# Optimization experiments

Hardware: AMD Instinct MI355X
Metric: run time of the kernel (lower is better)

The kernel has to match this reference:

```python
import jax, jax.numpy as jnp
import numpy as np

R, C, DIN, E, NREG = 1024, 8192, 16, 5, 2048

def setup_inputs() -> dict:
    key = jax.random.key(0)
    k1, k2, k3, k4, k5 = jax.random.split(key, 5)
    return {
        "region_cell_embedding": jax.random.normal(k1, (R, C, DIN), dtype=jnp.float32),
        "regions_oi": jax.random.randint(k2, (R,), 0, NREG, dtype=jnp.int64),
        "W1": jax.random.normal(k3, (NREG, DIN, E), dtype=jnp.float32) / np.sqrt(DIN),
        "b1": jax.random.normal(k4, (NREG, E), dtype=jnp.float32) * 0.1,
        "Wf": jax.random.normal(k5, (NREG, E, 1), dtype=jnp.float32) / np.sqrt(E),
    }

def reference(region_cell_embedding, regions_oi, W1, b1, Wf):
    # region_cell_embedding: [R, C, DIN]; each region r uses weights W1[regions_oi[r]]
    w = W1[regions_oi]                      # [R, DIN, E] gathered per-region weights
    b = b1[regions_oi]                      # [R, E]
    h = jnp.einsum('rci,rie->rce', region_cell_embedding, w) + b[:, None, :]
    h = jax.nn.gelu(h, approximate=False)   # torch.nn.GELU default is exact (erf)
    wf = Wf[regions_oi]                     # [R, E, 1], final MultiLinear has no bias
    out = jnp.einsum('rce,reo->rco', h, wf)[..., 0]  # [R, C]
    return out.T                            # [C, R] (cells x regions)
```

## Files before the change

### kernel.cpp

```cpp
#include <hip/hip_runtime.h>
#include <math.h>

#define RDIM 1024
#define CDIM 8192
#define DIN  16
#define EDIM 5

#define RT   16
#define CT   256
#define WROW 96

__device__ __forceinline__ float gelu_fast(float x) {
    float x2 = x * x;
    float w  = fmaf(0.044715f, x2, 1.0f);
    float t  = x * w;
    float e  = __builtin_amdgcn_exp2f(-2.3022078f * t);
    float s  = __builtin_amdgcn_rcpf(1.0f + e);
    return x * s;
}

__global__ __launch_bounds__(256)
void e2e_kernel(const float* __restrict__ emb,
                const int*   __restrict__ gidx,
                const float* __restrict__ W1,
                const float* __restrict__ b1,
                const float* __restrict__ Wf,
                float* __restrict__ out)
{
    __shared__ int   s_g[RT];
    __shared__ float s_w[RT * WROW];
    __shared__ float s_tile[CT * (RT + 1)];

    const int tid = threadIdx.x;
    const int c0  = blockIdx.x * CT;
    const int r0  = blockIdx.y * RT;

    if (tid < RT) s_g[tid] = gidx[r0 + tid];
    __syncthreads();

    for (int idx = tid; idx < RT * 90; idx += 256) {
        int rl = idx / 90;
        int k  = idx - rl * 90;
        int g  = s_g[rl];
        float v; int dst;
        if (k < 80)      { v = W1[g * 80 + k];       dst = k;     }
        else if (k < 85) { v = b1[g * 5 + (k - 80)]; dst = k;     }
        else             { v = Wf[g * 5 + (k - 85)]; dst = k + 3; }
        s_w[rl * WROW + dst] = v;
    }
    __syncthreads();

    const int lane = tid & 63;
    const int wv   = tid >> 6;

    #pragma unroll 1
    for (int q = 0; q < 4; ++q) {
        const int rl = wv * 4 + q;
        const int r  = r0 + rl;

        const float4* wp = (const float4*)(s_w + rl * WROW);
        float ww[80], bb[EDIM], wf[EDIM];
        #pragma unroll
        for (int q4 = 0; q4 < 20; ++q4) ((float4*)ww)[q4] = wp[q4];
        {
            float4 bt = wp[20];
            bb[0] = bt.x; bb[1] = bt.y; bb[2] = bt.z; bb[3] = bt.w;
            bb[4] = s_w[rl * WROW + 84];
            float4 ft = wp[22];
            wf[0] = ft.x; wf[1] = ft.y; wf[2] = ft.z; wf[3] = ft.w;
            wf[4] = s_w[rl * WROW + 92];
        }

        #pragma unroll
        for (int m = 0; m < 4; ++m) {
            const int cl = lane + 64 * m;
            const int c  = c0 + cl;
            const float4* p = (const float4*)(emb + ((size_t)r * CDIM + c) * DIN);
            float4 x0 = p[0], x1 = p[1], x2 = p[2], x3 = p[3];
            float x[DIN] = { x0.x, x0.y, x0.z, x0.w,
                             x1.x, x1.y, x1.z, x1.w,
                             x2.x, x2.y, x2.z, x2.w,
                             x3.x, x3.y, x3.z, x3.w };
            float acc = 0.f;
            #pragma unroll
            for (int e = 0; e < EDIM; ++e) {
                float h = bb[e];
                #pragma unroll
                for (int i = 0; i < DIN; ++i)
                    h = fmaf(x[i], ww[i * EDIM + e], h);
                h = gelu_fast(h);
                acc = fmaf(h, wf[e], acc);
            }
            s_tile[cl * (RT + 1) + rl] = acc;
        }
    }
    __syncthreads();

    const int orl  = tid & 15;
    const int ocl0 = tid >> 4;
    #pragma unroll
    for (int it = 0; it < 16; ++it) {
        const int cl = ocl0 + 16 * it;
        out[(size_t)(c0 + cl) * RDIM + r0 + orl] = s_tile[cl * (RT + 1) + orl];
    }
}

extern "C" void kernel_launch(void* const* d_in, const int* in_sizes, int n_in,
                              void* d_out, int out_size, void* d_ws, size_t ws_size,
                              hipStream_t stream) {
    const float* emb  = (const float*)d_in[0];
    const int*   gidx = (const int*)d_in[1];
    const float* W1   = (const float*)d_in[2];
    const float* b1   = (const float*)d_in[3];
    const float* Wf   = (const float*)d_in[4];
    float* out = (float*)d_out;

    dim3 grid(CDIM / CT, RDIM / RT);
    dim3 block(256);
    e2e_kernel<<<grid, block, 0, stream>>>(emb, gidx, W1, b1, Wf, out);
}
```

Before: 819.4 us.

## Split each cell's input across four lanes with float4 coalesced loads and shuffle reduction

Each cell's 16-element input is now spread across four lanes, each loading one float4, so consecutive lanes read consecutive memory. Partial dot products are combined with cross-lane shuffles, and each lane keeps only 20 weights instead of 80. This targets uncoalesced strided loads and high register pressure. In exchange it adds shuffles and computes GELU redundantly on four lanes per cell.

```diff
diff --git a/kernel.cpp b/kernel.cpp
--- a/kernel.cpp
+++ b/kernel.cpp
@@ -1,5 +1,4 @@
 #include <hip/hip_runtime.h>
-#include <math.h>
 
 #define RDIM 1024
 #define CDIM 8192
@@ -12,8 +11,7 @@
 
 __device__ __forceinline__ float gelu_fast(float x) {
     float x2 = x * x;
-    float w  = fmaf(0.044715f, x2, 1.0f);
-    float t  = x * w;
+    float t  = x * fmaf(0.044715f, x2, 1.0f);
     float e  = __builtin_amdgcn_exp2f(-2.3022078f * t);
     float s  = __builtin_amdgcn_rcpf(1.0f + e);
     return x * s;
@@ -52,46 +50,51 @@
 
     const int lane = tid & 63;
     const int wv   = tid >> 6;
+    const int q4   = lane & 3;
+    const int quad = lane >> 2;
 
     #pragma unroll 1
     for (int q = 0; q < 4; ++q) {
         const int rl = wv * 4 + q;
         const int r  = r0 + rl;
 
-        const float4* wp = (const float4*)(s_w + rl * WROW);
-        float ww[80], bb[EDIM], wf[EDIM];
+        const float4* wp4 = (const float4*)(s_w + rl * WROW + q4 * 20);
+        float wl[20];
         #pragma unroll
-        for (int q4 = 0; q4 < 20; ++q4) ((float4*)ww)[q4] = wp[q4];
+        for (int t = 0; t < 5; ++t) ((float4*)wl)[t] = wp4[t];
+        float bb[EDIM], wf[EDIM];
         {
-            float4 bt = wp[20];
+            const float* wr = s_w + rl * WROW;
+            float4 bt = *(const float4*)(wr + 80);
             bb[0] = bt.x; bb[1] = bt.y; bb[2] = bt.z; bb[3] = bt.w;
-            bb[4] = s_w[rl * WROW + 84];
-            float4 ft = wp[22];
+            bb[4] = wr[84];
+            float4 ft = *(const float4*)(wr + 88);
             wf[0] = ft.x; wf[1] = ft.y; wf[2] = ft.z; wf[3] = ft.w;
-            wf[4] = s_w[rl * WROW + 92];
+            wf[4] = wr[92];
         }
 
-        #pragma unroll
-        for (int m = 0; m < 4; ++m) {
-            const int cl = lane + 64 * m;
-            const int c  = c0 + cl;
-            const float4* p = (const float4*)(emb + ((size_t)r * CDIM + c) * DIN);
-            float4 x0 = p[0], x1 = p[1], x2 = p[2], x3 = p[3];
-            float x[DIN] = { x0.x, x0.y, x0.z, x0.w,
-                             x1.x, x1.y, x1.z, x1.w,
-                             x2.x, x2.y, x2.z, x2.w,
-                             x3.x, x3.y, x3.z, x3.w };
+        const float4* src = (const float4*)(emb + ((size_t)r * CDIM + c0) * DIN);
+
+        #pragma unroll 4
+        for (int j = 0; j < 16; ++j) {
+            float4 x4 = src[j * 64 + lane];
+            float part[EDIM];
+            #pragma unroll
+            for (int e = 0; e < EDIM; ++e)
+                part[e] = fmaf(x4.x, wl[e],
+                          fmaf(x4.y, wl[5 + e],
+                          fmaf(x4.z, wl[10 + e], x4.w * wl[15 + e])));
             float acc = 0.f;
             #pragma unroll
             for (int e = 0; e < EDIM; ++e) {
-                float h = bb[e];
-                #pragma unroll
-                for (int i = 0; i < DIN; ++i)
-                    h = fmaf(x[i], ww[i * EDIM + e], h);
-                h = gelu_fast(h);
-                acc = fmaf(h, wf[e], acc);
+                float v = part[e];
+                v += __shfl_xor(v, 1);
+                v += __shfl_xor(v, 2);
+                v += bb[e];
+                acc = fmaf(gelu_fast(v), wf[e], acc);
             }
-            s_tile[cl * (RT + 1) + rl] = acc;
+            if (q4 == 0)
+                s_tile[(j * 16 + quad) * (RT + 1) + rl] = acc;
         }
     }
     __syncthreads();
```

Result: faster. 735.1 us (-10.3%).
